# Kernel optimization log

Hardware: AMD Instinct MI355X
Metric: run time of the kernel (lower is better)

## Reference

```python
import jax, jax.numpy as jnp
import numpy as np

NUM_GROUPS = 8
EPS = 1e-5


def group_norm(x, gamma, beta):
    # x: [B, C, H, W]
    B, C, H, W = x.shape
    xg = x.reshape(B, NUM_GROUPS, C // NUM_GROUPS, H, W)
    mean = xg.mean(axis=(2, 3, 4), keepdims=True)
    var = xg.var(axis=(2, 3, 4), keepdims=True)
    xn = ((xg - mean) * jax.lax.rsqrt(var + EPS)).reshape(B, C, H, W)
    return xn * gamma[None, :, None, None] + beta[None, :, None, None]


def conv1x1(x, w, b):
    # x: [B, C, H, W], w: [Cout, Cin], b: [Cout]
    return jnp.einsum('bchw,oc->bohw', x, w) + b[None, :, None, None]


def setup_inputs() -> dict:
    key = jax.random.key(0)
    ks = jax.random.split(key, 7)
    C = 128
    x = jax.random.normal(ks[0], (4, C, 64, 64), dtype=jnp.float32)
    norm_w = jnp.ones((C,), dtype=jnp.float32)
    norm_b = jnp.zeros((C,), dtype=jnp.float32)
    s = 1.0 / np.sqrt(C)
    qkv_w = jax.random.normal(ks[1], (3 * C, C), dtype=jnp.float32) * s
    qkv_b = jax.random.normal(ks[2], (3 * C,), dtype=jnp.float32) * 0.01
    proj_w = jax.random.normal(ks[3], (C, C), dtype=jnp.float32) * s
    proj_b = jax.random.normal(ks[4], (C,), dtype=jnp.float32) * 0.01
    return {"x": x, "norm_w": norm_w, "norm_b": norm_b,
            "qkv_w": qkv_w, "qkv_b": qkv_b,
            "proj_w": proj_w, "proj_b": proj_b}


def reference(x, norm_w, norm_b, qkv_w, qkv_b, proj_w, proj_b):
    B, C, H, W = x.shape
    qkv = conv1x1(group_norm(x, norm_w, norm_b), qkv_w, qkv_b)
    q, k, v = jnp.split(qkv, 3, axis=1)           # each [B, C, H, W]
    q = q.reshape(B, C, H * W).transpose(0, 2, 1)  # [B, HW, C]
    k = k.reshape(B, C, H * W)                     # [B, C, HW]
    v = v.reshape(B, C, H * W).transpose(0, 2, 1)  # [B, HW, C]
    scale = 1.0 / np.sqrt(C).astype(np.float32)
    attn = jax.nn.softmax(jnp.einsum('bnc,bcm->bnm', q, k) * scale, axis=-1)
    out = jnp.einsum('bnm,bmc->bnc', attn, v)      # [B, HW, C]
    out = out.transpose(0, 2, 1).reshape(B, C, H, W)
    return x + conv1x1(out, proj_w, proj_b)
```

## Files before the change

### kernel.cpp

```cpp
#include <hip/hip_runtime.h>

typedef unsigned short u16;
typedef unsigned int   u32;

#define HW 4096
#define NC 128

typedef __bf16 bf16x8 __attribute__((ext_vector_type(8)));
typedef float  f32x16 __attribute__((ext_vector_type(16)));

__device__ __forceinline__ bf16x8 as_bf8(uint4 u){
    union { uint4 u; bf16x8 b; } c; c.u = u; return c.b;
}
__device__ __forceinline__ u32 pack2(float a, float b){
    return ((__float_as_uint(a) + 0x8000u) >> 16) | ((__float_as_uint(b) + 0x8000u) & 0xffff0000u);
}
__device__ __forceinline__ float bf_lo(u32 u){ return __uint_as_float(u << 16); }
__device__ __forceinline__ float bf_hi(u32 u){ return __uint_as_float(u & 0xffff0000u); }

__device__ __forceinline__ float exp2_hw(float x){ return __builtin_amdgcn_exp2f(x); }

__device__ __forceinline__ void plswap(u32 &a, u32 &b){
    asm("v_permlane32_swap_b32 %0, %1" : "+v"(a), "+v"(b));
}
__device__ __forceinline__ u32 cvtpk(float a, float b){
    u32 r; asm("v_cvt_pk_bf16_f32 %0, %1, %2" : "=v"(r) : "v"(a), "v"(b)); return r;
}

__global__ __launch_bounds__(256) void gnw_kernel(const float* __restrict__ x,
                                                  float* __restrict__ stats,
                                                  const float* __restrict__ qkv_w,
                                                  const float* __restrict__ proj_w,
                                                  uint4* __restrict__ Wf,
                                                  uint4* __restrict__ Pf){
    if (blockIdx.x < 256){
        int bg = blockIdx.x >> 3, part = blockIdx.x & 7;
        const float4* p = (const float4*)(x + (size_t)bg * 65536 + part * 8192);
        float s = 0.f, ss = 0.f;
        #pragma unroll
        for (int i = 0; i < 8; i++){
            float4 u = p[threadIdx.x + i*256];
            s  += u.x + u.y + u.z + u.w;
            ss += u.x*u.x + u.y*u.y + u.z*u.z + u.w*u.w;
        }
        #pragma unroll
        for (int off = 32; off > 0; off >>= 1){
            s  += __shfl_xor(s,  off);
            ss += __shfl_xor(ss, off);
        }
        __shared__ float rs[4], rss[4];
        int wid = threadIdx.x >> 6;
        if ((threadIdx.x & 63) == 0){ rs[wid] = s; rss[wid] = ss; }
        __syncthreads();
        if (threadIdx.x == 0){
            stats[bg*16 + part*2]     = rs[0]+rs[1]+rs[2]+rs[3];
            stats[bg*16 + part*2 + 1] = rss[0]+rss[1]+rss[2]+rss[3];
        }
    } else {
        int id = (blockIdx.x - 256)*256 + threadIdx.x;
        const float* src; uint4* dst; int fi;
        if (id < 6144){ src = qkv_w; dst = Wf; fi = id; }
        else          { src = proj_w; dst = Pf; fi = id - 6144; }
        int l = fi & 63, ks = (fi >> 6) & 7, ob = fi >> 9;
        int o = ob*32 + (l & 31);
        int c = ks*16 + ((l >> 5) << 3);
        const float* s = src + o*128 + c;
        dst[fi] = make_uint4(pack2(s[0],s[1]), pack2(s[2],s[3]), pack2(s[4],s[5]), pack2(s[6],s[7]));
    }
}

__global__ __launch_bounds__(256) void qkv_kernel(const float* __restrict__ x,
                                                  const float* __restrict__ stats,
                                                  const float* __restrict__ gamma,
                                                  const float* __restrict__ beta,
                                                  const uint4* __restrict__ Wf,
                                                  const float* __restrict__ bias,
                                                  uint4* __restrict__ Qf,
                                                  uint4* __restrict__ Kf,
                                                  uint4* __restrict__ Vf){
    __shared__ float gaL[128], beL[128], biasL[384];
    int b = blockIdx.x >> 7, tokblk = blockIdx.x & 127;
    int t = threadIdx.x, lane = t & 63, wv = t >> 6;
    if (t < 128){
        int g = t >> 4;
        float S = 0.f, SS = 0.f;
        #pragma unroll
        for (int p = 0; p < 8; p++){
            S  += stats[(b*8 + g)*16 + p*2];
            SS += stats[(b*8 + g)*16 + p*2 + 1];
        }
        float mean = S * (1.f/65536.f);
        float rstd = rsqrtf(SS * (1.f/65536.f) - mean*mean + 1e-5f);
        float ga = gamma[t] * rstd;
        gaL[t] = ga; beL[t] = beta[t] - mean*ga;
    }
    if (t < 192){ biasL[t] = bias[t]; biasL[t+192] = bias[t+192]; }
    __syncthreads();

    int h = lane >> 5, tl = lane & 31;
    uint4 xf[8];
    const float* xb = x + (size_t)b*128*HW + tokblk*32 + tl;
    #pragma unroll
    for (int ks = 0; ks < 8; ks++){
        int c0 = ks*16 + h*8;
        float4 g0 = *(float4*)&gaL[c0], g1 = *(float4*)&gaL[c0+4];
        float4 e0 = *(float4*)&beL[c0], e1 = *(float4*)&beL[c0+4];
        float v[8];
        #pragma unroll
        for (int j = 0; j < 8; j++) v[j] = xb[(size_t)(c0+j)*HW];
        v[0] = fmaf(v[0], g0.x, e0.x); v[1] = fmaf(v[1], g0.y, e0.y);
        v[2] = fmaf(v[2], g0.z, e0.z); v[3] = fmaf(v[3], g0.w, e0.w);
        v[4] = fmaf(v[4], g1.x, e1.x); v[5] = fmaf(v[5], g1.y, e1.y);
        v[6] = fmaf(v[6], g1.z, e1.z); v[7] = fmaf(v[7], g1.w, e1.w);
        xf[ks] = make_uint4(pack2(v[0],v[1]), pack2(v[2],v[3]), pack2(v[4],v[5]), pack2(v[6],v[7]));
    }

    bool up = (lane >= 32);
    #pragma unroll
    for (int i = 0; i < 3; i++){
        int ob = wv*3 + i;
        uint4 wf[8];
        #pragma unroll
        for (int ks = 0; ks < 8; ks++) wf[ks] = Wf[(ob*8 + ks)*64 + lane];
        f32x16 D;
        #pragma unroll
        for (int r = 0; r < 16; r++) D[r] = 0.f;
        if (ob < 8){
            #pragma unroll
            for (int ks = 0; ks < 8; ks++)
                D = __builtin_amdgcn_mfma_f32_32x32x16_bf16(as_bf8(wf[ks]), as_bf8(xf[ks]), D, 0,0,0);
            #pragma unroll
            for (int r = 0; r < 16; r++)
                D[r] += biasL[ob*32 + (r&3) + 8*(r>>2) + 4*h];
            u32 pk[8], xch[8];
            #pragma unroll
            for (int j = 0; j < 8; j++) pk[j] = pack2(D[2*j], D[2*j+1]);
            #pragma unroll
            for (int j = 0; j < 8; j++) xch[j] = __shfl_xor(pk[j], 32);
            uint4 F0 = up ? make_uint4(xch[2],xch[3],pk[2],pk[3]) : make_uint4(pk[0],pk[1],xch[0],xch[1]);
            uint4 F1 = up ? make_uint4(xch[6],xch[7],pk[6],pk[7]) : make_uint4(pk[4],pk[5],xch[4],xch[5]);
            uint4* dst = (ob < 4) ? Qf : Kf;
            int obl = ob & 3;
            size_t base = (((size_t)b*128 + tokblk)*8 + obl*2)*64 + lane;
            dst[base] = F0; dst[base + 64] = F1;
        } else {
            #pragma unroll
            for (int ks = 0; ks < 8; ks++)
                D = __builtin_amdgcn_mfma_f32_32x32x16_bf16(as_bf8(xf[ks]), as_bf8(wf[ks]), D, 0,0,0);
            int nb = ob - 8;
            float vb = biasL[256 + nb*32 + tl];
            #pragma unroll
            for (int r = 0; r < 16; r++) D[r] += vb;
            u32 pk[8], xch[8];
            #pragma unroll
            for (int j = 0; j < 8; j++) pk[j] = pack2(D[2*j], D[2*j+1]);
            #pragma unroll
            for (int j = 0; j < 8; j++) xch[j] = __shfl_xor(pk[j], 32);
            uint4 F0 = up ? make_uint4(xch[2],xch[3],pk[2],pk[3]) : make_uint4(pk[0],pk[1],xch[0],xch[1]);
            uint4 F1 = up ? make_uint4(xch[6],xch[7],pk[6],pk[7]) : make_uint4(pk[4],pk[5],xch[4],xch[5]);
            int it = tokblk >> 1, t2 = tokblk & 1;
            size_t base = ((((size_t)b*64 + it)*4 + nb)*4 + t2*2)*64 + lane;
            Vf[base] = F0; Vf[base + 64] = F1;
        }
    }
}

__global__ __launch_bounds__(256, 2) void attn_kernel(const uint4* __restrict__ Qf,
                                                      const uint4* __restrict__ Kf,
                                                      const uint4* __restrict__ Vf,
                                                      uint4* __restrict__ Opart,
                                                      float* __restrict__ lsum){
    __shared__ float fsm[8192];
    __shared__ float lred[64];
    int pair = blockIdx.x & 7, qx = blockIdx.x >> 3;
    int b = pair >> 1, ksp = pair & 1;
    int t = threadIdx.x, lane = t & 63, wv = t >> 6;
    int qh = wv >> 1, kh = wv & 1;
    const float SC2 = 0.12751744361402804f;
    const float B2  = -11.541560327111707f;

    uint4 qf[8];
    const uint4* qptr = Qf + (((size_t)b*128 + qx*2 + qh)*8)*64 + lane;
    #pragma unroll
    for (int ks = 0; ks < 8; ks++) qf[ks] = qptr[ks*64];

    f32x16 O[4];
    #pragma unroll
    for (int nb = 0; nb < 4; nb++)
        #pragma unroll
        for (int r = 0; r < 16; r++) O[nb][r] = 0.f;
    float l_i = 0.f;

    const uint4* kgw = Kf + (((size_t)b*128 + ksp*64)*8)*64 + (kh<<9) + lane;
    const uint4* vgw = Vf + (((size_t)b*64  + ksp*32)*16)*64 + (kh<<7) + lane;

    uint4 kf[8], vf[8];
    #pragma unroll
    for (int ks = 0; ks < 8; ks++) kf[ks] = kgw[ks*64];
    #pragma unroll
    for (int nb = 0; nb < 4; nb++){
        vf[nb*2]   = vgw[nb*256];
        vf[nb*2+1] = vgw[nb*256 + 64];
    }

    for (int it = 0; it < 32; it++){
        f32x16 Sa, Sb;
        #pragma unroll
        for (int r = 0; r < 16; r++){ Sa[r] = 0.f; Sb[r] = 0.f; }
        #pragma unroll
        for (int ks = 0; ks < 4; ks++)
            Sa = __builtin_amdgcn_mfma_f32_32x32x16_bf16(as_bf8(kf[ks]), as_bf8(qf[ks]), Sa, 0,0,0);
        #pragma unroll
        for (int ks = 4; ks < 8; ks++)
            Sb = __builtin_amdgcn_mfma_f32_32x32x16_bf16(as_bf8(kf[ks]), as_bf8(qf[ks]), Sb, 0,0,0);
        #pragma unroll
        for (int r = 0; r < 16; r++) Sa[r] += Sb[r];

        if (it < 31){
            const uint4* kn = kgw + (it+1)*1024;
            #pragma unroll
            for (int ks = 0; ks < 8; ks++) kf[ks] = kn[ks*64];
        }

        float psum = 0.f;
        u32 pk[8];
        #pragma unroll
        for (int q = 0; q < 4; q++){
            float e0 = exp2_hw(__fmaf_rn(Sa[q*4+0], SC2, B2));
            float e1 = exp2_hw(__fmaf_rn(Sa[q*4+1], SC2, B2));
            float e2 = exp2_hw(__fmaf_rn(Sa[q*4+2], SC2, B2));
            float e3 = exp2_hw(__fmaf_rn(Sa[q*4+3], SC2, B2));
            psum += (e0+e1)+(e2+e3);
            pk[2*q] = cvtpk(e0,e1); pk[2*q+1] = cvtpk(e2,e3);
        }
        {
            u32 ua = __float_as_uint(psum), ub = ua;
            plswap(ua, ub);
            l_i += __uint_as_float(ua) + __uint_as_float(ub);
        }

        plswap(pk[0], pk[2]); plswap(pk[1], pk[3]);
        plswap(pk[4], pk[6]); plswap(pk[5], pk[7]);
        uint4 fr0 = make_uint4(pk[0], pk[1], pk[2], pk[3]);
        uint4 fr1 = make_uint4(pk[4], pk[5], pk[6], pk[7]);

        #pragma unroll
        for (int nb = 0; nb < 4; nb++){
            O[nb] = __builtin_amdgcn_mfma_f32_32x32x16_bf16(as_bf8(vf[nb*2]),   as_bf8(fr0), O[nb], 0,0,0);
            O[nb] = __builtin_amdgcn_mfma_f32_32x32x16_bf16(as_bf8(vf[nb*2+1]), as_bf8(fr1), O[nb], 0,0,0);
        }

        if (it < 31){
            const uint4* vn = vgw + (it+1)*1024;
            #pragma unroll
            for (int nb = 0; nb < 4; nb++){
                vf[nb*2]   = vn[nb*256];
                vf[nb*2+1] = vn[nb*256 + 64];
            }
        }
    }

    if (kh == 1){
        #pragma unroll
        for (int nb = 0; nb < 4; nb++)
            #pragma unroll
            for (int r = 0; r < 16; r++)
                fsm[((qh*4+nb)*16 + r)*64 + lane] = O[nb][r];
        if (lane < 32) lred[qh*32 + lane] = l_i;
    }
    __syncthreads();
    if (kh == 0){
        float lt = l_i + lred[qh*32 + (lane & 31)];
        if (lane < 32) lsum[((size_t)(ksp*4 + b))*HW + (qx*2+qh)*32 + lane] = lt;
        bool up = (lane >= 32);
        uint4* oc = Opart + (size_t)ksp*262144 + (((size_t)b*128 + qx*2 + qh)*8)*64 + lane;
        #pragma unroll
        for (int nb = 0; nb < 4; nb++){
            #pragma unroll
            for (int r = 0; r < 16; r++) O[nb][r] += fsm[((qh*4+nb)*16 + r)*64 + lane];
            u32 pk[8], xch[8];
            #pragma unroll
            for (int j = 0; j < 8; j++) pk[j] = pack2(O[nb][2*j], O[nb][2*j+1]);
            #pragma unroll
            for (int j = 0; j < 8; j++) xch[j] = __shfl_xor(pk[j], 32);
            uint4 F0 = up ? make_uint4(xch[2],xch[3],pk[2],pk[3]) : make_uint4(pk[0],pk[1],xch[0],xch[1]);
            uint4 F1 = up ? make_uint4(xch[6],xch[7],pk[6],pk[7]) : make_uint4(pk[4],pk[5],xch[4],xch[5]);
            oc[(nb*2)*64]     = F0;
            oc[(nb*2 + 1)*64] = F1;
        }
    }
}

__global__ __launch_bounds__(256) void proj_kernel(const uint4* __restrict__ Op,
                                                   const float* __restrict__ lsum,
                                                   const uint4* __restrict__ Pf,
                                                   const float* __restrict__ bias,
                                                   const float* __restrict__ x,
                                                   float* __restrict__ out){
    __shared__ uint4 ofL[1024];
    __shared__ float biasL[128];
    int t = threadIdx.x, lane = t & 63, ob = t >> 6;
    int b = blockIdx.x >> 7, tokblk = blockIdx.x & 127;
    int h = lane >> 5, tl = lane & 31;

    {
        size_t base0 = ((size_t)b*128 + tokblk)*512;
        #pragma unroll
        for (int i = 0; i < 2; i++) ofL[i*256 + t]       = Op[base0 + i*256 + t];
        #pragma unroll
        for (int i = 0; i < 2; i++) ofL[512 + i*256 + t] = Op[262144 + base0 + i*256 + t];
    }
    if (t < 128) biasL[t] = bias[t];

    int rowg = b*HW + tokblk*32 + tl;
    float inv = 1.f / (lsum[rowg] + lsum[16384 + rowg]);

    uint4 pf[8];
    #pragma unroll
    for (int ks = 0; ks < 8; ks++) pf[ks] = Pf[(ob*8 + ks)*64 + lane];

    __syncthreads();

    f32x16 D;
    #pragma unroll
    for (int r = 0; r < 16; r++) D[r] = 0.f;
    #pragma unroll
    for (int ks = 0; ks < 8; ks++)
        D = __builtin_amdgcn_mfma_f32_32x32x16_bf16(as_bf8(pf[ks]), as_bf8(ofL[ks*64 + lane]), D, 0,0,0);
    #pragma unroll
    for (int ks = 0; ks < 8; ks++)
        D = __builtin_amdgcn_mfma_f32_32x32x16_bf16(as_bf8(pf[ks]), as_bf8(ofL[512 + ks*64 + lane]), D, 0,0,0);

    #pragma unroll
    for (int r = 0; r < 16; r++){
        int o = ob*32 + (r&3) + 8*(r>>2) + 4*h;
        size_t gi = ((size_t)b*128 + o)*HW + tokblk*32 + tl;
        out[gi] = x[gi] + biasL[o] + D[r]*inv;
    }
}

extern "C" void kernel_launch(void* const* d_in, const int* in_sizes, int n_in,
                              void* d_out, int out_size, void* d_ws, size_t ws_size,
                              hipStream_t stream){
    const float* x      = (const float*)d_in[0];
    const float* norm_w = (const float*)d_in[1];
    const float* norm_b = (const float*)d_in[2];
    const float* qkv_w  = (const float*)d_in[3];
    const float* qkv_b  = (const float*)d_in[4];
    const float* proj_w = (const float*)d_in[5];
    const float* proj_b = (const float*)d_in[6];
    float* out = (float*)d_out;

    char* w = (char*)d_ws;
    float* stats = (float*)w;
    uint4* Qf   = (uint4*)(w + 2048);
    uint4* Kf   = (uint4*)(w + 4196352);
    uint4* Vf   = (uint4*)(w + 8390656);
    float* lsum = (float*)(w + 12584960);
    uint4* Wf   = (uint4*)(w + 12716032);
    uint4* Pf   = (uint4*)(w + 12814336);
    uint4* Op2  = (uint4*)(w + 12847104);

    gnw_kernel<<<288, 256, 0, stream>>>(x, stats, qkv_w, proj_w, Wf, Pf);
    qkv_kernel<<<512, 256, 0, stream>>>(x, stats, norm_w, norm_b, Wf, qkv_b, Qf, Kf, Vf);
    attn_kernel<<<512, 256, 0, stream>>>(Qf, Kf, Vf, Op2, lsum);
    proj_kernel<<<512, 256, 0, stream>>>(Op2, lsum, Pf, proj_b, x, out);
}
```

Baseline: 127.7 us.

## Fuse output projection into attention kernel via last-arriver atomic counter

Removes the separate projection kernel launch. Each attention block bumps a per-(batch, query-tile) atomic counter after writing its partial output, and the second of the two key-split blocks reads both partials from global memory and does the projection, residual add and bias for its 64 tokens. The counter is zeroed in the qkv kernel. This saves one launch and the tail gap between kernels, but adds fences and an atomic, and puts the projection work on half the blocks at the end of the attention kernel.

```diff
diff --git a/kernel.cpp b/kernel.cpp
--- a/kernel.cpp
+++ b/kernel.cpp
@@ -77,10 +77,12 @@
                                                   const float* __restrict__ bias,
                                                   uint4* __restrict__ Qf,
                                                   uint4* __restrict__ Kf,
-                                                  uint4* __restrict__ Vf){
+                                                  uint4* __restrict__ Vf,
+                                                  u32* __restrict__ cnt){
     __shared__ float gaL[128], beL[128], biasL[384];
     int b = blockIdx.x >> 7, tokblk = blockIdx.x & 127;
     int t = threadIdx.x, lane = t & 63, wv = t >> 6;
+    if (blockIdx.x == 0) cnt[t] = 0;
     if (t < 128){
         int g = t >> 4;
         float S = 0.f, SS = 0.f;
@@ -169,9 +171,16 @@
                                                       const uint4* __restrict__ Kf,
                                                       const uint4* __restrict__ Vf,
                                                       uint4* __restrict__ Opart,
-                                                      float* __restrict__ lsum){
+                                                      float* __restrict__ lsum,
+                                                      const uint4* __restrict__ Pf,
+                                                      const float* __restrict__ pbias,
+                                                      const float* __restrict__ x,
+                                                      float* __restrict__ out,
+                                                      u32* __restrict__ cnt){
     __shared__ float fsm[8192];
     __shared__ float lred[64];
+    __shared__ float biasP[128];
+    __shared__ int   winflag;
     int pair = blockIdx.x & 7, qx = blockIdx.x >> 3;
     int b = pair >> 1, ksp = pair & 1;
     int t = threadIdx.x, lane = t & 63, wv = t >> 6;
@@ -289,53 +298,48 @@
             oc[(nb*2 + 1)*64] = F1;
         }
     }
-}
-
-__global__ __launch_bounds__(256) void proj_kernel(const uint4* __restrict__ Op,
-                                                   const float* __restrict__ lsum,
-                                                   const uint4* __restrict__ Pf,
-                                                   const float* __restrict__ bias,
-                                                   const float* __restrict__ x,
-                                                   float* __restrict__ out){
-    __shared__ uint4 ofL[1024];
-    __shared__ float biasL[128];
-    int t = threadIdx.x, lane = t & 63, ob = t >> 6;
-    int b = blockIdx.x >> 7, tokblk = blockIdx.x & 127;
-    int h = lane >> 5, tl = lane & 31;
-
-    {
-        size_t base0 = ((size_t)b*128 + tokblk)*512;
-        #pragma unroll
-        for (int i = 0; i < 2; i++) ofL[i*256 + t]       = Op[base0 + i*256 + t];
-        #pragma unroll
-        for (int i = 0; i < 2; i++) ofL[512 + i*256 + t] = Op[262144 + base0 + i*256 + t];
-    }
-    if (t < 128) biasL[t] = bias[t];
-
-    int rowg = b*HW + tokblk*32 + tl;
-    float inv = 1.f / (lsum[rowg] + lsum[16384 + rowg]);
-
+
+    __threadfence();
+    __syncthreads();
+    if (t == 0) winflag = (atomicAdd(&cnt[b*64 + qx], 1u) == 1u);
+    __syncthreads();
+    if (!winflag) return;
+    __threadfence();
+
+    uint4* ofL = (uint4*)fsm;
+    size_t base0 = ((size_t)b*128 + qx*2)*512;
+    #pragma unroll
+    for (int i = 0; i < 4; i++) ofL[i*256 + t]        = Opart[base0 + i*256 + t];
+    #pragma unroll
+    for (int i = 0; i < 4; i++) ofL[1024 + i*256 + t] = Opart[262144 + base0 + i*256 + t];
+    if (t < 128) biasP[t] = pbias[t];
+    __syncthreads();
+
+    int ob = wv, h = lane >> 5, tl = lane & 31;
     uint4 pf[8];
     #pragma unroll
     for (int ks = 0; ks < 8; ks++) pf[ks] = Pf[(ob*8 + ks)*64 + lane];
 
-    __syncthreads();
-
-    f32x16 D;
-    #pragma unroll
-    for (int r = 0; r < 16; r++) D[r] = 0.f;
-    #pragma unroll
-    for (int ks = 0; ks < 8; ks++)
-        D = __builtin_amdgcn_mfma_f32_32x32x16_bf16(as_bf8(pf[ks]), as_bf8(ofL[ks*64 + lane]), D, 0,0,0);
-    #pragma unroll
-    for (int ks = 0; ks < 8; ks++)
-        D = __builtin_amdgcn_mfma_f32_32x32x16_bf16(as_bf8(pf[ks]), as_bf8(ofL[512 + ks*64 + lane]), D, 0,0,0);
-
-    #pragma unroll
-    for (int r = 0; r < 16; r++){
-        int o = ob*32 + (r&3) + 8*(r>>2) + 4*h;
-        size_t gi = ((size_t)b*128 + o)*HW + tokblk*32 + tl;
-        out[gi] = x[gi] + biasL[o] + D[r]*inv;
+    #pragma unroll
+    for (int tb = 0; tb < 2; tb++){
+        int tokblk = qx*2 + tb;
+        int rowg = b*HW + tokblk*32 + tl;
+        float inv = 1.f / (lsum[rowg] + lsum[16384 + rowg]);
+        f32x16 D;
+        #pragma unroll
+        for (int r = 0; r < 16; r++) D[r] = 0.f;
+        #pragma unroll
+        for (int ks = 0; ks < 8; ks++)
+            D = __builtin_amdgcn_mfma_f32_32x32x16_bf16(as_bf8(pf[ks]), as_bf8(ofL[tb*512 + ks*64 + lane]), D, 0,0,0);
+        #pragma unroll
+        for (int ks = 0; ks < 8; ks++)
+            D = __builtin_amdgcn_mfma_f32_32x32x16_bf16(as_bf8(pf[ks]), as_bf8(ofL[1024 + tb*512 + ks*64 + lane]), D, 0,0,0);
+        #pragma unroll
+        for (int r = 0; r < 16; r++){
+            int o = ob*32 + (r&3) + 8*(r>>2) + 4*h;
+            size_t gi = ((size_t)b*128 + o)*HW + tokblk*32 + tl;
+            out[gi] = x[gi] + biasP[o] + D[r]*inv;
+        }
     }
 }
 
@@ -360,9 +364,9 @@
     uint4* Wf   = (uint4*)(w + 12716032);
     uint4* Pf   = (uint4*)(w + 12814336);
     uint4* Op2  = (uint4*)(w + 12847104);
+    u32*   cnt  = (u32*)  (w + 21235712);
 
     gnw_kernel<<<288, 256, 0, stream>>>(x, stats, qkv_w, proj_w, Wf, Pf);
-    qkv_kernel<<<512, 256, 0, stream>>>(x, stats, norm_w, norm_b, Wf, qkv_b, Qf, Kf, Vf);
-    attn_kernel<<<512, 256, 0, stream>>>(Qf, Kf, Vf, Op2, lsum);
-    proj_kernel<<<512, 256, 0, stream>>>(Op2, lsum, Pf, proj_b, x, out);
-}
+    qkv_kernel<<<512, 256, 0, stream>>>(x, stats, norm_w, norm_b, Wf, qkv_b, Qf, Kf, Vf, cnt);
+    attn_kernel<<<512, 256, 0, stream>>>(Qf, Kf, Vf, Op2, lsum, Pf, proj_b, x, out, cnt);
+}
```

Measured after the change: 225.7 us. 76.7% more time.
